# Optimization experiments

Hardware: AMD Instinct MI355X
Metric: run time of the kernel (lower is better)

Reference implementation:

```python
import jax, jax.numpy as jnp
import numpy as np

N, E, D, H, C, TD, MD = 50000, 500000, 128, 2, 64, 32, 64


def setup_inputs() -> dict:
    key = jax.random.key(0)
    ks = jax.random.split(key, 16)
    s = 0.05
    return {
        "x": jax.random.normal(ks[0], (N, D), jnp.float32),
        "edge_index": jax.random.randint(ks[1], (2, E), 0, N, dtype=jnp.int64),
        "edge_time": jax.random.randint(ks[2], (E,), 0, 86400, dtype=jnp.int64),
        "msg": jax.random.normal(ks[3], (E, MD), jnp.float32),
        "Wt": jax.random.normal(ks[4], (1, TD), jnp.float32) * s,
        "bt": jax.random.normal(ks[5], (TD,), jnp.float32) * s,
        "Wq": jax.random.normal(ks[6], (D, H * C), jnp.float32) * s,
        "bq": jax.random.normal(ks[7], (H * C,), jnp.float32) * s,
        "Wk": jax.random.normal(ks[8], (D, H * C), jnp.float32) * s,
        "bk": jax.random.normal(ks[9], (H * C,), jnp.float32) * s,
        "Wv": jax.random.normal(ks[10], (D, H * C), jnp.float32) * s,
        "bv": jax.random.normal(ks[11], (H * C,), jnp.float32) * s,
        "We": jax.random.normal(ks[12], (TD + MD, H * C), jnp.float32) * s,
        "Wskip": jax.random.normal(ks[13], (D, H * C), jnp.float32) * s,
        "bskip": jax.random.normal(ks[14], (H * C,), jnp.float32) * s,
    }


def reference(x, edge_index, edge_time, msg, Wt, bt, Wq, bq, Wk, bk, Wv, bv, We, Wskip, bskip):
    n = x.shape[0]
    src, dst = edge_index[0], edge_index[1]

    # TGN-style time encoding: cos(Linear(t))  -> [E, TD]
    t = edge_time.astype(x.dtype)[:, None]
    rel_t = jnp.cos(t @ Wt + bt)
    edge_attr = jnp.concatenate([rel_t, msg], axis=-1)  # [E, TD+MD]

    # TransformerConv projections, reshaped to [n, H, C] then gathered per edge
    q = (x @ Wq + bq).reshape(n, H, C)[dst]   # [E, H, C]
    k = (x @ Wk + bk).reshape(n, H, C)[src]   # [E, H, C]
    v = (x @ Wv + bv).reshape(n, H, C)[src]   # [E, H, C]
    e = (edge_attr @ We).reshape(-1, H, C)    # [E, H, C]

    k = k + e
    alpha = (q * k).sum(-1) / jnp.sqrt(jnp.asarray(C, x.dtype))  # [E, H]

    # segment softmax over incoming edges of each dst node
    amax = jax.ops.segment_max(alpha, dst, num_segments=n)       # [n, H]
    amax = jnp.where(jnp.isfinite(amax), amax, 0.0)
    ex = jnp.exp(alpha - amax[dst])
    denom = jax.ops.segment_sum(ex, dst, num_segments=n)
    alpha = ex / (denom[dst] + 1e-16)                            # [E, H]

    out_e = (v + e) * alpha[..., None]                           # [E, H, C]
    out = jax.ops.segment_sum(out_e, dst, num_segments=n).reshape(n, H * C)

    # root/skip connection
    out = out + x @ Wskip + bskip
    return out
```

## Files before the change

kernel.cpp:

```cpp
#include <hip/hip_runtime.h>
#include <hip/hip_bf16.h>

#define NN 50000
#define NE 500000
#define DD 128
#define HCC 128
#define TDD 32
#define MDD 64

typedef __hip_bfloat16 bf16;
typedef _Float16 f16;
typedef __attribute__((ext_vector_type(8))) _Float16 f16x8;
typedef __attribute__((ext_vector_type(2))) _Float16 f16x2;
typedef __attribute__((ext_vector_type(4))) float f32x4;

__device__ __forceinline__ float2 bf2x(unsigned u) {
    union { unsigned v; float f; } a, b;
    a.v = u << 16; b.v = u & 0xffff0000u;
    float2 r; r.x = a.f; r.y = b.f; return r;
}

__global__ __launch_bounds__(256) void conv_x_kernel(
    const float* __restrict__ x, f16* __restrict__ xh)
{
    int i = blockIdx.x * 256 + threadIdx.x;
    if (i >= NN * DD / 4) return;
    float4 v = ((const float4*)x)[i];
    f16 o[4] = { (f16)v.x, (f16)v.y, (f16)v.z, (f16)v.w };
    *(uint2*)&xh[(size_t)i * 4] = *(uint2*)o;
}

__global__ __launch_bounds__(256) void conv_w_kernel(
    const float* __restrict__ Wq, const float* __restrict__ Wk,
    const float* __restrict__ Wv, const float* __restrict__ Wsk,
    const float* __restrict__ We,
    f16* __restrict__ WTh, f16* __restrict__ Weh, int* __restrict__ cnt)
{
    int idx = blockIdx.x * 256 + threadIdx.x;
    if (idx < 512 * 128) {
        int n = idx >> 7, k = idx & 127;
        int mat = n >> 7, col = n & 127;
        const float* W = (mat == 0) ? Wq : (mat == 1) ? Wk : (mat == 2) ? Wv : Wsk;
        WTh[idx] = (f16)W[k * 128 + col];
    } else if (idx < 512 * 128 + 96 * 128) {
        int i = idx - 512 * 128;
        Weh[i] = (f16)We[i];
    } else if (idx < 512 * 128 + 96 * 128 + NN) {
        cnt[idx - (512 * 128 + 96 * 128)] = 0;
    }
}

__global__ __launch_bounds__(256) void node_proj_kernel(
    const f16* __restrict__ xh, const f16* __restrict__ WTh,
    const float* __restrict__ bq, const float* __restrict__ bk,
    const float* __restrict__ bv, const float* __restrict__ bsk,
    f16* __restrict__ qh, f16* __restrict__ kh, f16* __restrict__ vh,
    float* __restrict__ outp)
{
    __shared__ f16 xs[64 * 136];
    __shared__ f16 ws[128 * 136];

    const int node0 = blockIdx.x * 64;
    const int g = blockIdx.y;

    for (int i = threadIdx.x; i < 64 * 32; i += 256) {
        int node = i >> 5, koff = (i & 31) * 4;
        int gn = node0 + node;
        uint2 val = {0u, 0u};
        if (gn < NN) val = *(const uint2*)&xh[(size_t)gn * DD + koff];
        *(uint2*)&xs[node * 136 + koff] = val;
    }
    const f16* wt = WTh + (size_t)g * 128 * 128;
    for (int i = threadIdx.x; i < 128 * 32; i += 256) {
        int n = i >> 5, koff = (i & 31) * 4;
        *(uint2*)&ws[n * 136 + koff] = *(const uint2*)&wt[n * 128 + koff];
    }
    __syncthreads();

    const int wave = threadIdx.x >> 6;
    const int lane = threadIdx.x & 63;
    const int m0 = wave * 16;
    const int lrow = lane & 15;
    const int lk = (lane >> 4) * 8;

    f32x4 acc[8];
    #pragma unroll
    for (int t = 0; t < 8; t++) acc[t] = (f32x4){0.f, 0.f, 0.f, 0.f};

    #pragma unroll
    for (int kc = 0; kc < 4; kc++) {
        f16x8 a = *(const f16x8*)&xs[(m0 + lrow) * 136 + kc * 32 + lk];
        #pragma unroll
        for (int t = 0; t < 8; t++) {
            f16x8 b = *(const f16x8*)&ws[(t * 16 + lrow) * 136 + kc * 32 + lk];
            acc[t] = __builtin_amdgcn_mfma_f32_16x16x32_f16(a, b, acc[t], 0, 0, 0);
        }
    }

    const float* bias = (g == 0) ? bq : (g == 1) ? bk : (g == 2) ? bv : bsk;
    f16* outh = (g == 0) ? qh : (g == 1) ? kh : vh;

    #pragma unroll 1
    for (int t = 0; t < 8; t++) {
        int col = t * 16 + lrow;
        float bc = bias[col];
        #pragma unroll
        for (int r = 0; r < 4; r++) {
            int node = node0 + m0 + (lane >> 4) * 4 + r;
            if (node < NN) {
                float val = acc[t][r] + bc;
                if (g < 3) outh[(size_t)node * HCC + col] = (f16)val;
                else       outp[(size_t)node * HCC + col] = val;
            }
        }
    }
}

__global__ __launch_bounds__(256) void g_kernel(
    const f16* __restrict__ qh, const f16* __restrict__ Weh,
    bf16* __restrict__ G)
{
    __shared__ f16 qs[64 * 136];
    __shared__ f16 ws[96 * 136];

    const int node0 = blockIdx.x * 64;
    for (int i = threadIdx.x; i < 64 * 32; i += 256) {
        int node = i >> 5, koff = (i & 31) * 4;
        int gn = node0 + node;
        uint2 val = {0u, 0u};
        if (gn < NN) val = *(const uint2*)&qh[(size_t)gn * DD + koff];
        *(uint2*)&qs[node * 136 + koff] = val;
    }
    for (int i = threadIdx.x; i < 96 * 32; i += 256) {
        int j = i >> 5, koff = (i & 31) * 4;
        *(uint2*)&ws[j * 136 + koff] = *(const uint2*)&Weh[j * 128 + koff];
    }
    __syncthreads();

    const int wave = threadIdx.x >> 6;
    const int lane = threadIdx.x & 63;
    const int m0 = wave * 16;
    const int lrow = lane & 15;
    const int lk = (lane >> 4) * 8;

    f16x8 afr[4];
    #pragma unroll
    for (int hk = 0; hk < 4; hk++) {
        int h = hk >> 1, kc = hk & 1;
        afr[hk] = *(const f16x8*)&qs[(m0 + lrow) * 136 + h * 64 + kc * 32 + lk];
    }

    f32x4 acc[12];
    #pragma unroll
    for (int t = 0; t < 12; t++) acc[t] = (f32x4){0.f, 0.f, 0.f, 0.f};

    #pragma unroll
    for (int t = 0; t < 12; t++) {
        int h = (t < 6) ? 0 : 1;
        int jt = (t < 6) ? t : t - 6;
        #pragma unroll
        for (int kc = 0; kc < 2; kc++) {
            f16x8 b = *(const f16x8*)&ws[(jt * 16 + lrow) * 136 + h * 64 + kc * 32 + lk];
            acc[t] = __builtin_amdgcn_mfma_f32_16x16x32_f16(afr[h * 2 + kc], b, acc[t], 0, 0, 0);
        }
    }

    #pragma unroll 1
    for (int t = 0; t < 12; t++) {
        int h = (t < 6) ? 0 : 1;
        int jt = (t < 6) ? t : t - 6;
        int col = h * 96 + jt * 16 + lrow;
        #pragma unroll
        for (int r = 0; r < 4; r++) {
            int node = node0 + m0 + (lane >> 4) * 4 + r;
            if (node < NN) G[(size_t)node * 192 + col] = __float2bfloat16(acc[t][r]);
        }
    }
}

__global__ __launch_bounds__(256) void hist_kernel(
    const int* __restrict__ ei, int* __restrict__ cnt)
{
    int gid = blockIdx.x * 256 + threadIdx.x;
    if (gid < NE) atomicAdd(&cnt[ei[NE + gid]], 1);
}

__global__ __launch_bounds__(256) void scan_a_kernel(
    const int* __restrict__ cnt, int* __restrict__ bsum)
{
    __shared__ int red[256];
    int gid = blockIdx.x * 256 + threadIdx.x;
    red[threadIdx.x] = (gid < NN) ? cnt[gid] : 0;
    __syncthreads();
    for (int off = 128; off > 0; off >>= 1) {
        if (threadIdx.x < off) red[threadIdx.x] += red[threadIdx.x + off];
        __syncthreads();
    }
    if (threadIdx.x == 0) bsum[blockIdx.x] = red[0];
}

__global__ __launch_bounds__(256) void scan_b_kernel(
    const int* __restrict__ bsum, int* __restrict__ boff, int* __restrict__ seg)
{
    __shared__ int s[256];
    int t = threadIdx.x;
    s[t] = (t < 196) ? bsum[t] : 0;
    __syncthreads();
    if (t == 0) {
        int run = 0;
        for (int b = 0; b < 196; b++) { int v = s[b]; s[b] = run; run += v; }
        seg[NN] = NE;
    }
    __syncthreads();
    if (t < 196) boff[t] = s[t];
}

__global__ __launch_bounds__(256) void scan_c_kernel(
    const int* __restrict__ cnt, const int* __restrict__ boff,
    int* __restrict__ seg, int* __restrict__ cur)
{
    __shared__ int s[256];
    int gid = blockIdx.x * 256 + threadIdx.x;
    int v = (gid < NN) ? cnt[gid] : 0;
    s[threadIdx.x] = v;
    __syncthreads();
    for (int off = 1; off < 256; off <<= 1) {
        int t = (threadIdx.x >= off) ? s[threadIdx.x - off] : 0;
        __syncthreads();
        s[threadIdx.x] += t;
        __syncthreads();
    }
    int excl = s[threadIdx.x] - v + boff[blockIdx.x];
    if (gid < NN) { seg[gid] = excl; cur[gid] = excl; }
}

__global__ __launch_bounds__(256) void scatter_kernel(
    const int* __restrict__ ei, const int* __restrict__ et,
    int* __restrict__ cur, int* __restrict__ perm,
    int* __restrict__ esrc, int* __restrict__ edst, float* __restrict__ etim)
{
    int gid = blockIdx.x * 256 + threadIdx.x;
    if (gid < NE) {
        int d = ei[NE + gid];
        int pos = atomicAdd(&cur[d], 1);
        perm[pos] = gid;
        esrc[pos] = ei[gid];
        edst[pos] = d;
        etim[pos] = (float)et[gid];
    }
}

__global__ __launch_bounds__(256) void edge_fused_kernel(
    const float* __restrict__ msg, const int* __restrict__ perm,
    const int* __restrict__ esrc, const int* __restrict__ edst,
    const float* __restrict__ etim,
    const float* __restrict__ Wt, const float* __restrict__ bt,
    const f16* __restrict__ qh, const f16* __restrict__ kh,
    const bf16* __restrict__ G,
    bf16* __restrict__ emsg, float2* __restrict__ exv)
{
    __shared__ float wt_s[TDD], bt_s[TDD];
    if (threadIdx.x < TDD) {
        wt_s[threadIdx.x] = Wt[threadIdx.x];
        bt_s[threadIdx.x] = bt[threadIdx.x];
    }
    __syncthreads();

    size_t idx = (size_t)blockIdx.x * 256 + threadIdx.x;
    if (idx >= (size_t)NE * 8) return;
    int i = (int)(idx >> 3);
    int sub = (int)(idx & 7);

    int src = esrc[i], dst = edst[i];
    float t = etim[i];
    int pe = perm[i];

    const float4* mrow = (const float4*)(msg + ((size_t)pe << 6));
    float4 v0 = mrow[sub * 2];
    float4 v1 = mrow[sub * 2 + 1];
    bf16 o[8] = { __float2bfloat16(v0.x), __float2bfloat16(v0.y),
                  __float2bfloat16(v0.z), __float2bfloat16(v0.w),
                  __float2bfloat16(v1.x), __float2bfloat16(v1.y),
                  __float2bfloat16(v1.z), __float2bfloat16(v1.w) };
    *(uint4*)&emsg[((size_t)i << 6) + sub * 8] = *(uint4*)o;

    union U16 { uint4 u; f16x2 h[4]; };
    const f16* qrow = qh + (size_t)dst * DD;
    const f16* krow = kh + (size_t)src * DD;
    U16 q0, k0, q1, k1;
    q0.u = *(const uint4*)(qrow + 8 * sub);
    k0.u = *(const uint4*)(krow + 8 * sub);
    q1.u = *(const uint4*)(qrow + 64 + 8 * sub);
    k1.u = *(const uint4*)(krow + 64 + 8 * sub);
    float s0 = 0.f, s1 = 0.f;
    #pragma unroll
    for (int j = 0; j < 4; j++) {
#if defined(__has_builtin) && __has_builtin(__builtin_amdgcn_fdot2)
        s0 = __builtin_amdgcn_fdot2(q0.h[j], k0.h[j], s0, false);
        s1 = __builtin_amdgcn_fdot2(q1.h[j], k1.h[j], s1, false);
#else
        s0 = fmaf((float)q0.h[j][0], (float)k0.h[j][0], s0);
        s0 = fmaf((float)q0.h[j][1], (float)k0.h[j][1], s0);
        s1 = fmaf((float)q1.h[j][0], (float)k1.h[j][0], s1);
        s1 = fmaf((float)q1.h[j][1], (float)k1.h[j][1], s1);
#endif
    }

    const bf16* grow = G + (size_t)dst * 192;

    uint2 gc0 = *(const uint2*)(grow + 4 * sub);
    uint2 gc1 = *(const uint2*)(grow + 96 + 4 * sub);
    float cj[4];
    #pragma unroll
    for (int j = 0; j < 4; j++)
        cj[j] = __cosf(fmaf(t, wt_s[4 * sub + j], bt_s[4 * sub + j]));
    {
        float2 p;
        p = bf2x(gc0.x); s0 = fmaf(cj[0], p.x, s0); s0 = fmaf(cj[1], p.y, s0);
        p = bf2x(gc0.y); s0 = fmaf(cj[2], p.x, s0); s0 = fmaf(cj[3], p.y, s0);
        p = bf2x(gc1.x); s1 = fmaf(cj[0], p.x, s1); s1 = fmaf(cj[1], p.y, s1);
        p = bf2x(gc1.y); s1 = fmaf(cj[2], p.x, s1); s1 = fmaf(cj[3], p.y, s1);
    }

    uint4 gm0 = *(const uint4*)(grow + 32 + 8 * sub);
    uint4 gm1 = *(const uint4*)(grow + 128 + 8 * sub);
    {
        float2 p;
        p = bf2x(gm0.x); s0 = fmaf(v0.x, p.x, s0); s0 = fmaf(v0.y, p.y, s0);
        p = bf2x(gm0.y); s0 = fmaf(v0.z, p.x, s0); s0 = fmaf(v0.w, p.y, s0);
        p = bf2x(gm0.z); s0 = fmaf(v1.x, p.x, s0); s0 = fmaf(v1.y, p.y, s0);
        p = bf2x(gm0.w); s0 = fmaf(v1.z, p.x, s0); s0 = fmaf(v1.w, p.y, s0);
        p = bf2x(gm1.x); s1 = fmaf(v0.x, p.x, s1); s1 = fmaf(v0.y, p.y, s1);
        p = bf2x(gm1.y); s1 = fmaf(v0.z, p.x, s1); s1 = fmaf(v0.w, p.y, s1);
        p = bf2x(gm1.z); s1 = fmaf(v1.x, p.x, s1); s1 = fmaf(v1.y, p.y, s1);
        p = bf2x(gm1.w); s1 = fmaf(v1.z, p.x, s1); s1 = fmaf(v1.w, p.y, s1);
    }

    #pragma unroll
    for (int off = 1; off < 8; off <<= 1) {
        s0 += __shfl_xor(s0, off);
        s1 += __shfl_xor(s1, off);
    }
    if (sub == 0) {
        float2 ex;
        ex.x = __expf(s0 * 0.125f);
        ex.y = __expf(s1 * 0.125f);
        exv[i] = ex;
    }
}

__global__ __launch_bounds__(256) void agg_kernel(
    const int* __restrict__ esrc, const float* __restrict__ etim,
    const bf16* __restrict__ emsg,
    const float* __restrict__ Wt, const float* __restrict__ bt,
    const f16* __restrict__ vh, const float2* __restrict__ exv,
    const int* __restrict__ seg,
    float* __restrict__ Sv, float* __restrict__ dnv,
    float* __restrict__ outp)
{
    __shared__ float wt_s[TDD], bt_s[TDD];
    if (threadIdx.x < TDD) {
        wt_s[threadIdx.x] = Wt[threadIdx.x];
        bt_s[threadIdx.x] = bt[threadIdx.x];
    }
    __syncthreads();

    const int lane = threadIdx.x & 63;
    const int gw = blockIdx.x * 4 + (threadIdx.x >> 6);
    const int NW = gridDim.x * 4;
    const bool half0 = (lane < 32);
    const float wtv = wt_s[lane & 31];
    const float btv = bt_s[lane & 31];
    const int mcol = half0 ? (32 + lane) : (lane - 32);

    for (int n = gw; n < NN; n += NW) {
        const int s0 = seg[n], s1 = seg[n + 1];

        float2 acc; acc.x = 0.f; acc.y = 0.f;
        float accd = 0.f;
        float s00 = 0.f, s01 = 0.f, s10 = 0.f, s11 = 0.f;

        int i = s0;
        #pragma unroll 1
        for (; i + 4 <= s1; i += 4) {
            int srcu[4]; float2 exu[4]; float ttu[4]; float mgu[4]; f16x2 vvu[4];
            #pragma unroll
            for (int u = 0; u < 4; u++) {
                srcu[u] = esrc[i + u];
                exu[u]  = exv[i + u];
                ttu[u]  = etim[i + u];
                mgu[u]  = __bfloat162float(emsg[((size_t)(i + u) << 6) + mcol]);
            }
            #pragma unroll
            for (int u = 0; u < 4; u++)
                vvu[u] = *(const f16x2*)&vh[(size_t)srcu[u] * HCC + 2 * lane];
            #pragma unroll
            for (int u = 0; u < 4; u++) {
                float cs = __cosf(fmaf(ttu[u], wtv, btv));
                float r0 = half0 ? cs : mgu[u];
                float r1 = half0 ? mgu[u] : 0.f;
                float exh = half0 ? exu[u].x : exu[u].y;
                acc.x = fmaf(exh, (float)vvu[u][0], acc.x);
                acc.y = fmaf(exh, (float)vvu[u][1], acc.y);
                accd += exh;
                s00 = fmaf(exu[u].x, r0, s00); s01 = fmaf(exu[u].x, r1, s01);
                s10 = fmaf(exu[u].y, r0, s10); s11 = fmaf(exu[u].y, r1, s11);
            }
        }
        #pragma unroll 1
        for (; i < s1; i++) {
            int src = esrc[i];
            float2 ex = exv[i];
            float tt = etim[i];
            float mg = __bfloat162float(emsg[((size_t)i << 6) + mcol]);
            f16x2 v2 = *(const f16x2*)&vh[(size_t)src * HCC + 2 * lane];
            float cs = __cosf(fmaf(tt, wtv, btv));
            float r0 = half0 ? cs : mg;
            float r1 = half0 ? mg : 0.f;
            float exh = half0 ? ex.x : ex.y;
            acc.x = fmaf(exh, (float)v2[0], acc.x);
            acc.y = fmaf(exh, (float)v2[1], acc.y);
            accd += exh;
            s00 = fmaf(ex.x, r0, s00); s01 = fmaf(ex.x, r1, s01);
            s10 = fmaf(ex.y, r0, s10); s11 = fmaf(ex.y, r1, s11);
        }

        float dn = accd + 1e-16f;
        size_t sb = (size_t)n * 192;
        Sv[sb + lane]      = s00;
        Sv[sb + 96 + lane] = s10;
        if (half0) {
            Sv[sb + 64 + lane]  = s01;
            Sv[sb + 160 + lane] = s11;
        }
        if ((lane & 31) == 0) dnv[n * 2 + (lane >> 5)] = accd;

        size_t nb = (size_t)n * HCC + 2 * lane;
        float2 sk = *(const float2*)&outp[nb];
        float2 o;
        o.x = acc.x / dn + sk.x;
        o.y = acc.y / dn + sk.y;
        *(float2*)&outp[nb] = o;
    }
}

__global__ __launch_bounds__(256) void epi_kernel(
    const float* __restrict__ Sv, const float* __restrict__ dnv,
    const float* __restrict__ We, float* __restrict__ outp)
{
    __shared__ float st[192 * 36];
    const int node0 = blockIdx.x * 32;
    for (int idx = threadIdx.x; idx < 32 * 192; idx += 256) {
        int n = idx / 192, c = idx - n * 192;
        int node = node0 + n;
        st[c * 36 + n] = (node < NN) ? Sv[(size_t)node * 192 + c] : 0.f;
    }
    __syncthreads();

    const int wave = threadIdx.x >> 6;
    const int lane = threadIdx.x & 63;
    const int nb = wave * 8;
    const int hoff = (lane < 32) ? 0 : 96;
    const float2* We2 = (const float2*)We;

    float a[8][2];
    #pragma unroll
    for (int n = 0; n < 8; n++) { a[n][0] = 0.f; a[n][1] = 0.f; }

    #pragma unroll 8
    for (int j = 0; j < 96; j++) {
        float2 w = We2[j * 64 + lane];
        const float* sr = &st[(hoff + j) * 36 + nb];
        float sv[8];
        *(float4*)&sv[0] = *(const float4*)sr;
        *(float4*)&sv[4] = *(const float4*)(sr + 4);
        #pragma unroll
        for (int n = 0; n < 8; n++) {
            a[n][0] = fmaf(sv[n], w.x, a[n][0]);
            a[n][1] = fmaf(sv[n], w.y, a[n][1]);
        }
    }

    #pragma unroll 1
    for (int n = 0; n < 8; n++) {
        int node = node0 + nb + n;
        if (node >= NN) break;
        float dn = dnv[node * 2 + (lane >> 5)] + 1e-16f;
        size_t b = (size_t)node * HCC + 2 * lane;
        float2 o = *(const float2*)&outp[b];
        o.x += a[n][0] / dn;
        o.y += a[n][1] / dn;
        *(float2*)&outp[b] = o;
    }
}

extern "C" void kernel_launch(void* const* d_in, const int* in_sizes, int n_in,
                              void* d_out, int out_size, void* d_ws, size_t ws_size,
                              hipStream_t stream) {
    const float* x   = (const float*)d_in[0];
    const int* ei    = (const int*)d_in[1];
    const int* et    = (const int*)d_in[2];
    const float* msg = (const float*)d_in[3];
    const float* Wt  = (const float*)d_in[4];
    const float* bt  = (const float*)d_in[5];
    const float* Wq  = (const float*)d_in[6];
    const float* bq  = (const float*)d_in[7];
    const float* Wk  = (const float*)d_in[8];
    const float* bk  = (const float*)d_in[9];
    const float* Wv  = (const float*)d_in[10];
    const float* bv  = (const float*)d_in[11];
    const float* We  = (const float*)d_in[12];
    const float* Wsk = (const float*)d_in[13];
    const float* bsk = (const float*)d_in[14];

    const size_t nf = (size_t)NN * HCC;
    f16* xh      = (f16*)d_ws;
    f16* qh      = xh + nf;
    f16* kh      = qh + nf;
    f16* vh      = kh + nf;
    f16* WTh     = vh + nf;
    f16* Weh     = WTh + 512 * 128;
    bf16* G      = (bf16*)(Weh + 96 * 128);
    bf16* emsg   = G + (size_t)NN * 192;
    float2* exv  = (float2*)(emsg + (size_t)NE * MDD);
    float* etim  = (float*)(exv + NE);
    float* Sv    = etim + NE;
    float* dnv   = Sv + (size_t)NN * 192;
    int* cnt     = (int*)(dnv + (size_t)NN * 2);
    int* seg     = cnt + NN;
    int* cur     = seg + NN + 1;
    int* perm    = cur + NN;
    int* esrc    = perm + NE;
    int* edst    = esrc + NE;
    int* bsum    = edst + NE;
    int* boff    = bsum + 256;
    size_t need  = (size_t)((char*)(boff + 256) - (char*)d_ws);
    if (ws_size < need) return;

    float* outp = (float*)d_out;

    conv_x_kernel<<<(NN * DD / 4 + 255) / 256, 256, 0, stream>>>(x, xh);
    conv_w_kernel<<<(512 * 128 + 96 * 128 + NN + 255) / 256, 256, 0, stream>>>(
        Wq, Wk, Wv, Wsk, We, WTh, Weh, cnt);
    dim3 npgrid((NN + 63) / 64, 4);
    node_proj_kernel<<<npgrid, 256, 0, stream>>>(
        xh, WTh, bq, bk, bv, bsk, qh, kh, vh, outp);
    g_kernel<<<(NN + 63) / 64, 256, 0, stream>>>(qh, Weh, G);
    hist_kernel<<<(NE + 255) / 256, 256, 0, stream>>>(ei, cnt);
    scan_a_kernel<<<196, 256, 0, stream>>>(cnt, bsum);
    scan_b_kernel<<<1, 256, 0, stream>>>(bsum, boff, seg);
    scan_c_kernel<<<196, 256, 0, stream>>>(cnt, boff, seg, cur);
    scatter_kernel<<<(NE + 255) / 256, 256, 0, stream>>>(
        ei, et, cur, perm, esrc, edst, etim);
    edge_fused_kernel<<<(int)(((size_t)NE * 8 + 255) / 256), 256, 0, stream>>>(
        msg, perm, esrc, edst, etim, Wt, bt, qh, kh, G, emsg, exv);
    agg_kernel<<<3125, 256, 0, stream>>>(
        esrc, etim, emsg, Wt, bt, vh, exv, seg, Sv, dnv, outp);
    epi_kernel<<<(NN + 31) / 32, 256, 0, stream>>>(Sv, dnv, We, outp);
}
```

Measured before the change: 561.6 us.

## Fuse edge score computation into per-node aggregation and pack edge metadata

Removes the separate edge_fused kernel and its bf16 message copy and exp buffer. The aggregation wave now computes each edge's attention score inline (q·k plus the G terms via a 32-lane shuffle reduction) while accumulating. Scatter writes one packed int4 per edge (src, original id, time, dst) instead of four arrays. The x-to-fp16 conversion is folded into the node projection load, dropping a kernel. The cost is serialized shuffle reductions per edge inside the aggregation loop and extra k-row and fp32 msg gathers there.

```diff
diff --git a/kernel.cpp b/kernel.cpp
--- a/kernel.cpp
+++ b/kernel.cpp
@@ -18,16 +18,6 @@
     union { unsigned v; float f; } a, b;
     a.v = u << 16; b.v = u & 0xffff0000u;
     float2 r; r.x = a.f; r.y = b.f; return r;
-}
-
-__global__ __launch_bounds__(256) void conv_x_kernel(
-    const float* __restrict__ x, f16* __restrict__ xh)
-{
-    int i = blockIdx.x * 256 + threadIdx.x;
-    if (i >= NN * DD / 4) return;
-    float4 v = ((const float4*)x)[i];
-    f16 o[4] = { (f16)v.x, (f16)v.y, (f16)v.z, (f16)v.w };
-    *(uint2*)&xh[(size_t)i * 4] = *(uint2*)o;
 }
 
 __global__ __launch_bounds__(256) void conv_w_kernel(
@@ -51,7 +41,7 @@
 }
 
 __global__ __launch_bounds__(256) void node_proj_kernel(
-    const f16* __restrict__ xh, const f16* __restrict__ WTh,
+    const float* __restrict__ x, const f16* __restrict__ WTh,
     const float* __restrict__ bq, const float* __restrict__ bk,
     const float* __restrict__ bv, const float* __restrict__ bsk,
     f16* __restrict__ qh, f16* __restrict__ kh, f16* __restrict__ vh,
@@ -66,9 +56,12 @@
     for (int i = threadIdx.x; i < 64 * 32; i += 256) {
         int node = i >> 5, koff = (i & 31) * 4;
         int gn = node0 + node;
-        uint2 val = {0u, 0u};
-        if (gn < NN) val = *(const uint2*)&xh[(size_t)gn * DD + koff];
-        *(uint2*)&xs[node * 136 + koff] = val;
+        f16 o4[4] = { (f16)0.f, (f16)0.f, (f16)0.f, (f16)0.f };
+        if (gn < NN) {
+            float4 v = *(const float4*)&x[(size_t)gn * DD + koff];
+            o4[0] = (f16)v.x; o4[1] = (f16)v.y; o4[2] = (f16)v.z; o4[3] = (f16)v.w;
+        }
+        *(uint2*)&xs[node * 136 + koff] = *(uint2*)o4;
     }
     const f16* wt = WTh + (size_t)g * 128 * 128;
     for (int i = threadIdx.x; i < 128 * 32; i += 256) {
@@ -236,28 +229,29 @@
 
 __global__ __launch_bounds__(256) void scatter_kernel(
     const int* __restrict__ ei, const int* __restrict__ et,
-    int* __restrict__ cur, int* __restrict__ perm,
-    int* __restrict__ esrc, int* __restrict__ edst, float* __restrict__ etim)
+    int* __restrict__ cur, int4* __restrict__ epack)
 {
     int gid = blockIdx.x * 256 + threadIdx.x;
     if (gid < NE) {
         int d = ei[NE + gid];
         int pos = atomicAdd(&cur[d], 1);
-        perm[pos] = gid;
-        esrc[pos] = ei[gid];
-        edst[pos] = d;
-        etim[pos] = (float)et[gid];
-    }
-}
-
-__global__ __launch_bounds__(256) void edge_fused_kernel(
-    const float* __restrict__ msg, const int* __restrict__ perm,
-    const int* __restrict__ esrc, const int* __restrict__ edst,
-    const float* __restrict__ etim,
+        int4 p;
+        p.x = ei[gid];
+        p.y = gid;
+        p.z = __float_as_int((float)et[gid]);
+        p.w = d;
+        epack[pos] = p;
+    }
+}
+
+__global__ __launch_bounds__(256) void agg_kernel(
+    const int4* __restrict__ epack, const float* __restrict__ msg,
     const float* __restrict__ Wt, const float* __restrict__ bt,
     const f16* __restrict__ qh, const f16* __restrict__ kh,
-    const bf16* __restrict__ G,
-    bf16* __restrict__ emsg, float2* __restrict__ exv)
+    const f16* __restrict__ vh, const bf16* __restrict__ G,
+    const int* __restrict__ seg,
+    float* __restrict__ Sv, float* __restrict__ dnv,
+    float* __restrict__ outp)
 {
     __shared__ float wt_s[TDD], bt_s[TDD];
     if (threadIdx.x < TDD) {
@@ -266,174 +260,100 @@
     }
     __syncthreads();
 
-    size_t idx = (size_t)blockIdx.x * 256 + threadIdx.x;
-    if (idx >= (size_t)NE * 8) return;
-    int i = (int)(idx >> 3);
-    int sub = (int)(idx & 7);
-
-    int src = esrc[i], dst = edst[i];
-    float t = etim[i];
-    int pe = perm[i];
-
-    const float4* mrow = (const float4*)(msg + ((size_t)pe << 6));
-    float4 v0 = mrow[sub * 2];
-    float4 v1 = mrow[sub * 2 + 1];
-    bf16 o[8] = { __float2bfloat16(v0.x), __float2bfloat16(v0.y),
-                  __float2bfloat16(v0.z), __float2bfloat16(v0.w),
-                  __float2bfloat16(v1.x), __float2bfloat16(v1.y),
-                  __float2bfloat16(v1.z), __float2bfloat16(v1.w) };
-    *(uint4*)&emsg[((size_t)i << 6) + sub * 8] = *(uint4*)o;
-
-    union U16 { uint4 u; f16x2 h[4]; };
-    const f16* qrow = qh + (size_t)dst * DD;
-    const f16* krow = kh + (size_t)src * DD;
-    U16 q0, k0, q1, k1;
-    q0.u = *(const uint4*)(qrow + 8 * sub);
-    k0.u = *(const uint4*)(krow + 8 * sub);
-    q1.u = *(const uint4*)(qrow + 64 + 8 * sub);
-    k1.u = *(const uint4*)(krow + 64 + 8 * sub);
-    float s0 = 0.f, s1 = 0.f;
-    #pragma unroll
-    for (int j = 0; j < 4; j++) {
-#if defined(__has_builtin) && __has_builtin(__builtin_amdgcn_fdot2)
-        s0 = __builtin_amdgcn_fdot2(q0.h[j], k0.h[j], s0, false);
-        s1 = __builtin_amdgcn_fdot2(q1.h[j], k1.h[j], s1, false);
-#else
-        s0 = fmaf((float)q0.h[j][0], (float)k0.h[j][0], s0);
-        s0 = fmaf((float)q0.h[j][1], (float)k0.h[j][1], s0);
-        s1 = fmaf((float)q1.h[j][0], (float)k1.h[j][0], s1);
-        s1 = fmaf((float)q1.h[j][1], (float)k1.h[j][1], s1);
-#endif
-    }
-
-    const bf16* grow = G + (size_t)dst * 192;
-
-    uint2 gc0 = *(const uint2*)(grow + 4 * sub);
-    uint2 gc1 = *(const uint2*)(grow + 96 + 4 * sub);
-    float cj[4];
-    #pragma unroll
-    for (int j = 0; j < 4; j++)
-        cj[j] = __cosf(fmaf(t, wt_s[4 * sub + j], bt_s[4 * sub + j]));
-    {
-        float2 p;
-        p = bf2x(gc0.x); s0 = fmaf(cj[0], p.x, s0); s0 = fmaf(cj[1], p.y, s0);
-        p = bf2x(gc0.y); s0 = fmaf(cj[2], p.x, s0); s0 = fmaf(cj[3], p.y, s0);
-        p = bf2x(gc1.x); s1 = fmaf(cj[0], p.x, s1); s1 = fmaf(cj[1], p.y, s1);
-        p = bf2x(gc1.y); s1 = fmaf(cj[2], p.x, s1); s1 = fmaf(cj[3], p.y, s1);
-    }
-
-    uint4 gm0 = *(const uint4*)(grow + 32 + 8 * sub);
-    uint4 gm1 = *(const uint4*)(grow + 128 + 8 * sub);
-    {
-        float2 p;
-        p = bf2x(gm0.x); s0 = fmaf(v0.x, p.x, s0); s0 = fmaf(v0.y, p.y, s0);
-        p = bf2x(gm0.y); s0 = fmaf(v0.z, p.x, s0); s0 = fmaf(v0.w, p.y, s0);
-        p = bf2x(gm0.z); s0 = fmaf(v1.x, p.x, s0); s0 = fmaf(v1.y, p.y, s0);
-        p = bf2x(gm0.w); s0 = fmaf(v1.z, p.x, s0); s0 = fmaf(v1.w, p.y, s0);
-        p = bf2x(gm1.x); s1 = fmaf(v0.x, p.x, s1); s1 = fmaf(v0.y, p.y, s1);
-        p = bf2x(gm1.y); s1 = fmaf(v0.z, p.x, s1); s1 = fmaf(v0.w, p.y, s1);
-        p = bf2x(gm1.z); s1 = fmaf(v1.x, p.x, s1); s1 = fmaf(v1.y, p.y, s1);
-        p = bf2x(gm1.w); s1 = fmaf(v1.z, p.x, s1); s1 = fmaf(v1.w, p.y, s1);
-    }
-
-    #pragma unroll
-    for (int off = 1; off < 8; off <<= 1) {
-        s0 += __shfl_xor(s0, off);
-        s1 += __shfl_xor(s1, off);
-    }
-    if (sub == 0) {
-        float2 ex;
-        ex.x = __expf(s0 * 0.125f);
-        ex.y = __expf(s1 * 0.125f);
-        exv[i] = ex;
-    }
-}
-
-__global__ __launch_bounds__(256) void agg_kernel(
-    const int* __restrict__ esrc, const float* __restrict__ etim,
-    const bf16* __restrict__ emsg,
-    const float* __restrict__ Wt, const float* __restrict__ bt,
-    const f16* __restrict__ vh, const float2* __restrict__ exv,
-    const int* __restrict__ seg,
-    float* __restrict__ Sv, float* __restrict__ dnv,
-    float* __restrict__ outp)
-{
-    __shared__ float wt_s[TDD], bt_s[TDD];
-    if (threadIdx.x < TDD) {
-        wt_s[threadIdx.x] = Wt[threadIdx.x];
-        bt_s[threadIdx.x] = bt[threadIdx.x];
-    }
-    __syncthreads();
-
     const int lane = threadIdx.x & 63;
+    const int c = lane & 31;
+    const int h = lane >> 5;
+    const float wtv = wt_s[c];
+    const float btv = bt_s[c];
     const int gw = blockIdx.x * 4 + (threadIdx.x >> 6);
     const int NW = gridDim.x * 4;
-    const bool half0 = (lane < 32);
-    const float wtv = wt_s[lane & 31];
-    const float btv = bt_s[lane & 31];
-    const int mcol = half0 ? (32 + lane) : (lane - 32);
 
     for (int n = gw; n < NN; n += NW) {
         const int s0 = seg[n], s1 = seg[n + 1];
 
+        f16x2 q2 = *(const f16x2*)&qh[(size_t)n * DD + 2 * lane];
+        const bf16* grow = G + (size_t)n * 192 + 96 * h;
+        float Gc  = __bfloat162float(grow[c]);
+        float Gm0 = __bfloat162float(grow[32 + 2 * c]);
+        float Gm1 = __bfloat162float(grow[33 + 2 * c]);
+
         float2 acc; acc.x = 0.f; acc.y = 0.f;
-        float accd = 0.f;
-        float s00 = 0.f, s01 = 0.f, s10 = 0.f, s11 = 0.f;
+        float accd = 0.f, sc = 0.f, sm0 = 0.f, sm1 = 0.f;
 
         int i = s0;
         #pragma unroll 1
         for (; i + 4 <= s1; i += 4) {
-            int srcu[4]; float2 exu[4]; float ttu[4]; float mgu[4]; f16x2 vvu[4];
+            int4 e[4]; f16x2 k2[4], v2[4]; float2 m[4];
+            #pragma unroll
+            for (int u = 0; u < 4; u++) e[u] = epack[i + u];
             #pragma unroll
             for (int u = 0; u < 4; u++) {
-                srcu[u] = esrc[i + u];
-                exu[u]  = exv[i + u];
-                ttu[u]  = etim[i + u];
-                mgu[u]  = __bfloat162float(emsg[((size_t)(i + u) << 6) + mcol]);
+                int src = e[u].x;
+                k2[u] = *(const f16x2*)&kh[(size_t)src * HCC + 2 * lane];
+                v2[u] = *(const f16x2*)&vh[(size_t)src * HCC + 2 * lane];
+                m[u]  = *(const float2*)&msg[((size_t)e[u].y << 6) + 2 * c];
             }
             #pragma unroll
-            for (int u = 0; u < 4; u++)
-                vvu[u] = *(const f16x2*)&vh[(size_t)srcu[u] * HCC + 2 * lane];
-            #pragma unroll
             for (int u = 0; u < 4; u++) {
-                float cs = __cosf(fmaf(ttu[u], wtv, btv));
-                float r0 = half0 ? cs : mgu[u];
-                float r1 = half0 ? mgu[u] : 0.f;
-                float exh = half0 ? exu[u].x : exu[u].y;
-                acc.x = fmaf(exh, (float)vvu[u][0], acc.x);
-                acc.y = fmaf(exh, (float)vvu[u][1], acc.y);
-                accd += exh;
-                s00 = fmaf(exu[u].x, r0, s00); s01 = fmaf(exu[u].x, r1, s01);
-                s10 = fmaf(exu[u].y, r0, s10); s11 = fmaf(exu[u].y, r1, s11);
+                float t = __int_as_float(e[u].z);
+                float cs = __cosf(fmaf(t, wtv, btv));
+                float p = fmaf(cs, Gc, fmaf(m[u].x, Gm0, m[u].y * Gm1));
+#if defined(__has_builtin) && __has_builtin(__builtin_amdgcn_fdot2)
+                p = __builtin_amdgcn_fdot2(q2, k2[u], p, false);
+#else
+                p = fmaf((float)q2[0], (float)k2[u][0], p);
+                p = fmaf((float)q2[1], (float)k2[u][1], p);
+#endif
+                p += __shfl_xor(p, 1);
+                p += __shfl_xor(p, 2);
+                p += __shfl_xor(p, 4);
+                p += __shfl_xor(p, 8);
+                p += __shfl_xor(p, 16);
+                float ex = __expf(p * 0.125f);
+                acc.x = fmaf(ex, (float)v2[u][0], acc.x);
+                acc.y = fmaf(ex, (float)v2[u][1], acc.y);
+                accd += ex;
+                sc  = fmaf(ex, cs, sc);
+                sm0 = fmaf(ex, m[u].x, sm0);
+                sm1 = fmaf(ex, m[u].y, sm1);
             }
         }
         #pragma unroll 1
         for (; i < s1; i++) {
-            int src = esrc[i];
-            float2 ex = exv[i];
-            float tt = etim[i];
-            float mg = __bfloat162float(emsg[((size_t)i << 6) + mcol]);
+            int4 e = epack[i];
+            int src = e.x;
+            f16x2 k2 = *(const f16x2*)&kh[(size_t)src * HCC + 2 * lane];
             f16x2 v2 = *(const f16x2*)&vh[(size_t)src * HCC + 2 * lane];
-            float cs = __cosf(fmaf(tt, wtv, btv));
-            float r0 = half0 ? cs : mg;
-            float r1 = half0 ? mg : 0.f;
-            float exh = half0 ? ex.x : ex.y;
-            acc.x = fmaf(exh, (float)v2[0], acc.x);
-            acc.y = fmaf(exh, (float)v2[1], acc.y);
-            accd += exh;
-            s00 = fmaf(ex.x, r0, s00); s01 = fmaf(ex.x, r1, s01);
-            s10 = fmaf(ex.y, r0, s10); s11 = fmaf(ex.y, r1, s11);
+            float2 m = *(const float2*)&msg[((size_t)e.y << 6) + 2 * c];
+            float t = __int_as_float(e.z);
+            float cs = __cosf(fmaf(t, wtv, btv));
+            float p = fmaf(cs, Gc, fmaf(m.x, Gm0, m.y * Gm1));
+#if defined(__has_builtin) && __has_builtin(__builtin_amdgcn_fdot2)
+            p = __builtin_amdgcn_fdot2(q2, k2, p, false);
+#else
+            p = fmaf((float)q2[0], (float)k2[0], p);
+            p = fmaf((float)q2[1], (float)k2[1], p);
+#endif
+            p += __shfl_xor(p, 1);
+            p += __shfl_xor(p, 2);
+            p += __shfl_xor(p, 4);
+            p += __shfl_xor(p, 8);
+            p += __shfl_xor(p, 16);
+            float ex = __expf(p * 0.125f);
+            acc.x = fmaf(ex, (float)v2[0], acc.x);
+            acc.y = fmaf(ex, (float)v2[1], acc.y);
+            accd += ex;
+            sc  = fmaf(ex, cs, sc);
+            sm0 = fmaf(ex, m.x, sm0);
+            sm1 = fmaf(ex, m.y, sm1);
         }
 
         float dn = accd + 1e-16f;
-        size_t sb = (size_t)n * 192;
-        Sv[sb + lane]      = s00;
-        Sv[sb + 96 + lane] = s10;
-        if (half0) {
-            Sv[sb + 64 + lane]  = s01;
-            Sv[sb + 160 + lane] = s11;
-        }
-        if ((lane & 31) == 0) dnv[n * 2 + (lane >> 5)] = accd;
+        size_t sb = (size_t)n * 192 + 96 * h;
+        Sv[sb + c]          = sc;
+        Sv[sb + 32 + 2 * c] = sm0;
+        Sv[sb + 33 + 2 * c] = sm1;
+        if (c == 0) dnv[n * 2 + h] = accd;
 
         size_t nb = (size_t)n * HCC + 2 * lane;
         float2 sk = *(const float2*)&outp[nb];
@@ -514,47 +434,37 @@
     const float* bsk = (const float*)d_in[14];
 
     const size_t nf = (size_t)NN * HCC;
-    f16* xh      = (f16*)d_ws;
-    f16* qh      = xh + nf;
+    f16* qh      = (f16*)d_ws;
     f16* kh      = qh + nf;
     f16* vh      = kh + nf;
     f16* WTh     = vh + nf;
     f16* Weh     = WTh + 512 * 128;
     bf16* G      = (bf16*)(Weh + 96 * 128);
-    bf16* emsg   = G + (size_t)NN * 192;
-    float2* exv  = (float2*)(emsg + (size_t)NE * MDD);
-    float* etim  = (float*)(exv + NE);
-    float* Sv    = etim + NE;
+    float* Sv    = (float*)(G + (size_t)NN * 192);
     float* dnv   = Sv + (size_t)NN * 192;
-    int* cnt     = (int*)(dnv + (size_t)NN * 2);
+    int4* epack  = (int4*)(dnv + (size_t)NN * 2);
+    int* cnt     = (int*)(epack + NE);
     int* seg     = cnt + NN;
     int* cur     = seg + NN + 1;
-    int* perm    = cur + NN;
-    int* esrc    = perm + NE;
-    int* edst    = esrc + NE;
-    int* bsum    = edst + NE;
+    int* bsum    = cur + NN;
     int* boff    = bsum + 256;
     size_t need  = (size_t)((char*)(boff + 256) - (char*)d_ws);
     if (ws_size < need) return;
 
     float* outp = (float*)d_out;
 
-    conv_x_kernel<<<(NN * DD / 4 + 255) / 256, 256, 0, stream>>>(x, xh);
     conv_w_kernel<<<(512 * 128 + 96 * 128 + NN + 255) / 256, 256, 0, stream>>>(
         Wq, Wk, Wv, Wsk, We, WTh, Weh, cnt);
     dim3 npgrid((NN + 63) / 64, 4);
     node_proj_kernel<<<npgrid, 256, 0, stream>>>(
-        xh, WTh, bq, bk, bv, bsk, qh, kh, vh, outp);
+        x, WTh, bq, bk, bv, bsk, qh, kh, vh, outp);
     g_kernel<<<(NN + 63) / 64, 256, 0, stream>>>(qh, Weh, G);
     hist_kernel<<<(NE + 255) / 256, 256, 0, stream>>>(ei, cnt);
     scan_a_kernel<<<196, 256, 0, stream>>>(cnt, bsum);
     scan_b_kernel<<<1, 256, 0, stream>>>(bsum, boff, seg);
     scan_c_kernel<<<196, 256, 0, stream>>>(cnt, boff, seg, cur);
-    scatter_kernel<<<(NE + 255) / 256, 256, 0, stream>>>(
-        ei, et, cur, perm, esrc, edst, etim);
-    edge_fused_kernel<<<(int)(((size_t)NE * 8 + 255) / 256), 256, 0, stream>>>(
-        msg, perm, esrc, edst, etim, Wt, bt, qh, kh, G, emsg, exv);
+    scatter_kernel<<<(NE + 255) / 256, 256, 0, stream>>>(ei, et, cur, epack);
     agg_kernel<<<3125, 256, 0, stream>>>(
-        esrc, etim, emsg, Wt, bt, vh, exv, seg, Sv, dnv, outp);
+        epack, msg, Wt, bt, qh, kh, vh, G, seg, Sv, dnv, outp);
     epi_kernel<<<(NN + 31) / 32, 256, 0, stream>>>(Sv, dnv, We, outp);
 }
```

Measured after the change: 539.0 us. -4.0%, faster.
